# Kernel tuning notes

Measured on AMD Instinct MI355X. Metric: run time of the kernel, lower is better.

The kernel has to match this reference:

```python
import jax, jax.numpy as jnp
import numpy as np

N, E, D, H, OUT = 50000, 262144, 128, 256, 1
NUM_EXPERTS, TOP_K = 4, 1


def _mlp(x, w1, b1, w2, b2):
    return jnp.maximum(x @ w1 + b1, 0.0) @ w2 + b2


def setup_inputs() -> dict:
    key = jax.random.key(0)
    ks = jax.random.split(key, 16)
    def lin(k, fan_in, fan_out):
        bound = 1.0 / np.sqrt(fan_in)
        return jax.random.uniform(k, (fan_in, fan_out), jnp.float32, -bound, bound)
    return {
        "z": jax.random.normal(ks[0], (N, D), jnp.float32),
        "u": jax.random.randint(ks[1], (E,), 0, N, jnp.int64),
        "v": jax.random.randint(ks[2], (E,), 0, N, jnp.int64),
        "gate_w": lin(ks[3], 4 * D, NUM_EXPERTS),
        "gate_b": jnp.zeros((NUM_EXPERTS,), jnp.float32),
        "cat_w1": lin(ks[4], 2 * D, H), "cat_b1": jnp.zeros((H,), jnp.float32),
        "cat_w2": lin(ks[5], H, OUT), "cat_b2": jnp.zeros((OUT,), jnp.float32),
        "dist_w1": lin(ks[6], D, H), "dist_b1": jnp.zeros((H,), jnp.float32),
        "dist_w2": lin(ks[7], H, OUT), "dist_b2": jnp.zeros((OUT,), jnp.float32),
        "mul_w1": lin(ks[8], D, H), "mul_b1": jnp.zeros((H,), jnp.float32),
        "mul_w2": lin(ks[9], H, OUT), "mul_b2": jnp.zeros((OUT,), jnp.float32),
        "all_w1": lin(ks[10], 4 * D, H), "all_b1": jnp.zeros((H,), jnp.float32),
        "all_w2": lin(ks[11], H, OUT), "all_b2": jnp.zeros((OUT,), jnp.float32),
    }


def reference(z, u, v, gate_w, gate_b,
              cat_w1, cat_b1, cat_w2, cat_b2,
              dist_w1, dist_b1, dist_w2, dist_b2,
              mul_w1, mul_b1, mul_w2, mul_b2,
              all_w1, all_b1, all_w2, all_b2):
    z_u = z[u]                      # [E, D]
    z_v = z[v]                      # [E, D]
    z_cat = jnp.concatenate([z_u, z_v], axis=-1)        # [E, 2D]
    z_diff = jnp.abs(z_u - z_v)                         # [E, D]
    z_mul = z_u * z_v                                   # [E, D]
    edge_feat = jnp.concatenate([z_cat, z_diff, z_mul], axis=-1)  # [E, 4D]

    s1 = _mlp(z_cat, cat_w1, cat_b1, cat_w2, cat_b2)
    s2 = _mlp(z_diff, dist_w1, dist_b1, dist_w2, dist_b2)
    s3 = _mlp(z_mul, mul_w1, mul_b1, mul_w2, mul_b2)
    s4 = _mlp(edge_feat, all_w1, all_b1, all_w2, all_b2)
    scores = jnp.stack([s1, s2, s3, s4], axis=1)        # [E, 4, OUT]

    gate_logits = edge_feat @ gate_w + gate_b           # [E, 4]
    gate_probs = jax.nn.softmax(gate_logits, axis=-1)

    # top_k=1 with straight-through estimator (forward value == hard gate)
    topk_vals, topk_idx = jax.lax.top_k(gate_probs, TOP_K)
    hard_gate = jax.nn.one_hot(topk_idx[:, 0], NUM_EXPERTS, dtype=gate_probs.dtype) * topk_vals[:, :1]
    gate_st = hard_gate + gate_probs - jax.lax.stop_gradient(gate_probs)

    out = jnp.einsum("ek,eko->eo", gate_st, scores)     # [E, OUT]
    # dropout is identity in eval mode
    avg_expert_usage = gate_probs.mean(axis=0)
    aux_loss = (avg_expert_usage ** 2).sum() * NUM_EXPERTS
    return out, aux_loss
```

## Files before the change

kernel.cpp:

```cpp
#include <hip/hip_runtime.h>
#include <hip/hip_bf16.h>
#include <math.h>

#define N_NODES 50000
#define E_EDGES 262144
#define D_FEAT  128
#define H_HID   256
#define NEXP    4

typedef __attribute__((ext_vector_type(8))) short  short8;
typedef __attribute__((ext_vector_type(4))) float  floatx4;

#define W1B_OFF0 0
#define W1B_OFF1 65536
#define W1B_OFF2 98304
#define W1B_OFF3 131072
#define W1B_TOT  262144

__device__ __forceinline__ unsigned short f2bf(float f) {
    __hip_bfloat16 h = __float2bfloat16(f);
    return *reinterpret_cast<unsigned short*>(&h);
}

__global__ __launch_bounds__(256) void conv_kernel(
    const float* __restrict__ cw1, const float* __restrict__ dw1,
    const float* __restrict__ mw1, const float* __restrict__ aw1,
    unsigned short* __restrict__ w1b)
{
    int r = blockIdx.x;
    int n = threadIdx.x;
    const float* src; int k, off;
    if (r < 256)      { src = cw1; k = r;       off = W1B_OFF0; }
    else if (r < 384) { src = dw1; k = r - 256; off = W1B_OFF1; }
    else if (r < 512) { src = mw1; k = r - 384; off = W1B_OFF2; }
    else              { src = aw1; k = r - 512; off = W1B_OFF3; }
    w1b[off + (((k >> 3) * 256 + n) << 3) + (k & 7)] = f2bf(src[k * 256 + n]);
}

__global__ __launch_bounds__(256) void node_kernel(
    const float* __restrict__ z, const float* __restrict__ gw,
    double* __restrict__ nodeTab, double* __restrict__ gwd)
{
    int n = blockIdx.x * 256 + threadIdx.x;
    if (n < 128) {
        #pragma unroll
        for (int k = 0; k < 4; ++k) {
            gwd[n * 8 + k]     = (double)gw[4 * (256 + n) + k];
            gwd[n * 8 + 4 + k] = (double)gw[4 * (384 + n) + k];
        }
    }
    if (n >= N_NODES) return;

    const float4* zr = (const float4*)(z + (long)n * D_FEAT);
    double u0 = 0, u1 = 0, u2 = 0, u3 = 0;
    double v0 = 0, v1 = 0, v2 = 0, v3 = 0;
    for (int d4 = 0; d4 < D_FEAT / 4; ++d4) {
        float4 a = zr[d4];
        float av[4] = {a.x, a.y, a.z, a.w};
        #pragma unroll
        for (int j = 0; j < 4; ++j) {
            int d = d4 * 4 + j;
            const float4 g0 = *(const float4*)(gw + 4 * d);
            const float4 g1 = *(const float4*)(gw + 4 * (128 + d));
            double ad = (double)av[j];
            u0 += ad * (double)g0.x; u1 += ad * (double)g0.y;
            u2 += ad * (double)g0.z; u3 += ad * (double)g0.w;
            v0 += ad * (double)g1.x; v1 += ad * (double)g1.y;
            v2 += ad * (double)g1.z; v3 += ad * (double)g1.w;
        }
    }
    double* o = nodeTab + (long)n * 8;
    o[0] = u0; o[1] = u1; o[2] = u2; o[3] = u3;
    o[4] = v0; o[5] = v1; o[6] = v2; o[7] = v3;
}

__global__ __launch_bounds__(256) void gate_kernel(
    const float* __restrict__ z, const int* __restrict__ u, const int* __restrict__ v,
    const double* __restrict__ nodeTab, const double* __restrict__ gwd,
    const float* __restrict__ gb,
    float* __restrict__ probsum, unsigned* __restrict__ gcount,
    int* __restrict__ lists, float* __restrict__ pval)
{
    int tid  = threadIdx.x;
    int lane = tid & 63;
    int e    = blockIdx.x * 256 + tid;

    int ue = u[e], ve = v[e];
    const float4* zu4 = (const float4*)(z + (long)ue * D_FEAT);
    const float4* zv4 = (const float4*)(z + (long)ve * D_FEAT);
    const double* nu = nodeTab + (long)ue * 8;
    const double* nv = nodeTab + (long)ve * 8;

    double l0 = (double)gb[0] + nu[0] + nv[4];
    double l1 = (double)gb[1] + nu[1] + nv[5];
    double l2 = (double)gb[2] + nu[2] + nv[6];
    double l3 = (double)gb[3] + nu[3] + nv[7];

    for (int d4 = 0; d4 < D_FEAT / 4; ++d4) {
        float4 a = zu4[d4];
        float4 b = zv4[d4];
        float av[4] = {a.x, a.y, a.z, a.w};
        float bv[4] = {b.x, b.y, b.z, b.w};
        #pragma unroll
        for (int j = 0; j < 4; ++j) {
            int d = d4 * 4 + j;
            double ad = (double)fabsf(av[j] - bv[j]);
            double m  = (double)(av[j] * bv[j]);
            const double* gr = gwd + d * 8;
            l0 += ad * gr[0] + m * gr[4];
            l1 += ad * gr[1] + m * gr[5];
            l2 += ad * gr[2] + m * gr[6];
            l3 += ad * gr[3] + m * gr[7];
        }
    }

    int sel = 0;
    double lb = l0;
    if (l1 > lb) { lb = l1; sel = 1; }
    if (l2 > lb) { lb = l2; sel = 2; }
    if (l3 > lb) { lb = l3; sel = 3; }

    double mx = lb;
    float e0 = expf((float)(l0 - mx));
    float e1 = expf((float)(l1 - mx));
    float e2 = expf((float)(l2 - mx));
    float e3 = expf((float)(l3 - mx));
    float s  = e0 + e1 + e2 + e3;
    float inv = 1.0f / s;
    float p[4];
    p[0] = e0 * inv; p[1] = e1 * inv; p[2] = e2 * inv; p[3] = e3 * inv;
    float best = p[sel];

    __shared__ float s_ps[4];
    __shared__ int   s_cnt[4];
    __shared__ int   s_base[4];
    if (tid < 4) { s_ps[tid] = 0.0f; s_cnt[tid] = 0; }
    __syncthreads();

    float q0 = p[0], q1 = p[1], q2 = p[2], q3 = p[3];
    #pragma unroll
    for (int off = 32; off > 0; off >>= 1) {
        q0 += __shfl_down(q0, off);
        q1 += __shfl_down(q1, off);
        q2 += __shfl_down(q2, off);
        q3 += __shfl_down(q3, off);
    }
    if (lane == 0) {
        atomicAdd(&s_ps[0], q0); atomicAdd(&s_ps[1], q1);
        atomicAdd(&s_ps[2], q2); atomicAdd(&s_ps[3], q3);
    }

    unsigned long long lt = (lane == 0) ? 0ull : ((~0ull) >> (64 - lane));
    int mywb = 0, myrank = 0;
    #pragma unroll
    for (int k = 0; k < 4; ++k) {
        unsigned long long mask = __ballot(sel == k);
        if (mask) {
            int leader = (int)__ffsll((unsigned long long)mask) - 1;
            int wb = 0;
            if (lane == leader) wb = atomicAdd(&s_cnt[k], (int)__popcll(mask));
            wb = __shfl(wb, leader);
            if (sel == k) { mywb = wb; myrank = (int)__popcll(mask & lt); }
        }
    }
    __syncthreads();

    if (tid < 4) {
        s_base[tid] = (int)atomicAdd(&gcount[tid], (unsigned)s_cnt[tid]);
        atomicAdd(&probsum[tid], s_ps[tid]);
    }
    __syncthreads();

    int pos = s_base[sel] + mywb + myrank;
    lists[sel * E_EDGES + pos] = e;
    pval[e] = best;
}

#define FPAD 40
#define NCMAX 16

__global__ __launch_bounds__(256) void expert_kernel(
    const float* __restrict__ z, const int* __restrict__ u, const int* __restrict__ v,
    const unsigned short* __restrict__ w1b,
    const float* __restrict__ cb1, const float* __restrict__ cw2, const float* __restrict__ cb2,
    const float* __restrict__ db1, const float* __restrict__ dw2, const float* __restrict__ db2,
    const float* __restrict__ mb1, const float* __restrict__ mw2, const float* __restrict__ mb2,
    const float* __restrict__ ab1, const float* __restrict__ aw2, const float* __restrict__ ab2,
    const unsigned* __restrict__ gcount, const int* __restrict__ lists,
    const float* __restrict__ pval, float* __restrict__ out)
{
    int ex = blockIdx.y;
    const float *b1, *w2, *b2;
    int F, w1off;
    if (ex == 0)      { b1 = cb1; w2 = cw2; b2 = cb2; F = 256; w1off = W1B_OFF0; }
    else if (ex == 1) { b1 = db1; w2 = dw2; b2 = db2; F = 128; w1off = W1B_OFF1; }
    else if (ex == 2) { b1 = mb1; w2 = mw2; b2 = mb2; F = 128; w1off = W1B_OFF2; }
    else              { b1 = ab1; w2 = aw2; b2 = ab2; F = 512; w1off = W1B_OFF3; }

    unsigned cnt  = gcount[ex];
    unsigned tile = blockIdx.x * 32u;
    if (tile >= cnt) return;
    int nm = (int)min(32u, cnt - tile);

    __shared__ unsigned short featA[NCMAX][32][FPAD];
    __shared__ int   s_e[32], s_u[32], s_v[32];
    __shared__ float s_pv[32];
    __shared__ float red[4][32];

    int tid  = threadIdx.x;
    int wave = tid >> 6;
    int lane = tid & 63;
    int colA = lane & 15;
    int quad = lane >> 4;

    if (tid < 32) {
        int m = tid;
        int src = (m < nm) ? (int)(tile + m) : (int)tile;
        int e = lists[ex * E_EDGES + src];
        s_e[m] = e; s_u[m] = u[e]; s_v[m] = v[e]; s_pv[m] = pval[e];
    }
    __syncthreads();

    const short8* wB = (const short8*)(w1b + w1off);

    floatx4 acc[2][4];
    #pragma unroll
    for (int t = 0; t < 2; ++t)
        #pragma unroll
        for (int j = 0; j < 4; ++j)
            acc[t][j] = (floatx4)(0.0f);

    int fm = tid >> 3;
    int fk = (tid & 7) << 2;
    int nc = F >> 5;

    {
        const float* zu = z + (long)s_u[fm] * D_FEAT;
        const float* zv = z + (long)s_v[fm] * D_FEAT;
        for (int c = 0; c < nc; ++c) {
            int fg = c * 32 + fk;
            float4 val;
            if (ex == 0) {
                val = (fg < 128) ? *(const float4*)(zu + fg)
                                 : *(const float4*)(zv + fg - 128);
            } else if (ex == 1) {
                float4 a = *(const float4*)(zu + fg);
                float4 b = *(const float4*)(zv + fg);
                val.x = fabsf(a.x - b.x); val.y = fabsf(a.y - b.y);
                val.z = fabsf(a.z - b.z); val.w = fabsf(a.w - b.w);
            } else if (ex == 2) {
                float4 a = *(const float4*)(zu + fg);
                float4 b = *(const float4*)(zv + fg);
                val.x = a.x * b.x; val.y = a.y * b.y;
                val.z = a.z * b.z; val.w = a.w * b.w;
            } else {
                if (fg < 128) {
                    val = *(const float4*)(zu + fg);
                } else if (fg < 256) {
                    val = *(const float4*)(zv + fg - 128);
                } else if (fg < 384) {
                    float4 a = *(const float4*)(zu + fg - 256);
                    float4 b = *(const float4*)(zv + fg - 256);
                    val.x = fabsf(a.x - b.x); val.y = fabsf(a.y - b.y);
                    val.z = fabsf(a.z - b.z); val.w = fabsf(a.w - b.w);
                } else {
                    float4 a = *(const float4*)(zu + fg - 384);
                    float4 b = *(const float4*)(zv + fg - 384);
                    val.x = a.x * b.x; val.y = a.y * b.y;
                    val.z = a.z * b.z; val.w = a.w * b.w;
                }
            }
            ushort4 pk;
            pk.x = f2bf(val.x); pk.y = f2bf(val.y);
            pk.z = f2bf(val.z); pk.w = f2bf(val.w);
            *(ushort4*)(&featA[c][fm][fk]) = pk;
        }
    }
    __syncthreads();

    int nb = wave * 64 + colA;
    for (int c = 0; c < nc; ++c) {
        int g = c * 4 + quad;
        short8 bf0 = wB[g * 256 + nb +  0];
        short8 bf1 = wB[g * 256 + nb + 16];
        short8 bf2 = wB[g * 256 + nb + 32];
        short8 bf3 = wB[g * 256 + nb + 48];

        short8 a0 = *(const short8*)(&featA[c][colA][quad * 8]);
        short8 a1 = *(const short8*)(&featA[c][16 + colA][quad * 8]);

        acc[0][0] = __builtin_amdgcn_mfma_f32_16x16x32_bf16(a0, bf0, acc[0][0], 0, 0, 0);
        acc[1][0] = __builtin_amdgcn_mfma_f32_16x16x32_bf16(a1, bf0, acc[1][0], 0, 0, 0);
        acc[0][1] = __builtin_amdgcn_mfma_f32_16x16x32_bf16(a0, bf1, acc[0][1], 0, 0, 0);
        acc[1][1] = __builtin_amdgcn_mfma_f32_16x16x32_bf16(a1, bf1, acc[1][1], 0, 0, 0);
        acc[0][2] = __builtin_amdgcn_mfma_f32_16x16x32_bf16(a0, bf2, acc[0][2], 0, 0, 0);
        acc[1][2] = __builtin_amdgcn_mfma_f32_16x16x32_bf16(a1, bf2, acc[1][2], 0, 0, 0);
        acc[0][3] = __builtin_amdgcn_mfma_f32_16x16x32_bf16(a0, bf3, acc[0][3], 0, 0, 0);
        acc[1][3] = __builtin_amdgcn_mfma_f32_16x16x32_bf16(a1, bf3, acc[1][3], 0, 0, 0);
    }

    float b1v[4], w2v[4];
    #pragma unroll
    for (int j = 0; j < 4; ++j) {
        int h = wave * 64 + j * 16 + colA;
        b1v[j] = b1[h];
        w2v[j] = w2[h];
    }

    #pragma unroll
    for (int t = 0; t < 2; ++t) {
        #pragma unroll
        for (int r = 0; r < 4; ++r) {
            float s = 0.0f;
            #pragma unroll
            for (int j = 0; j < 4; ++j) {
                float h = acc[t][j][r] + b1v[j];
                s += fmaxf(h, 0.0f) * w2v[j];
            }
            s += __shfl_xor(s, 1);
            s += __shfl_xor(s, 2);
            s += __shfl_xor(s, 4);
            s += __shfl_xor(s, 8);
            if (colA == 0) {
                int m = 16 * t + quad * 4 + r;
                red[wave][m] = s;
            }
        }
    }
    __syncthreads();

    if (tid < 32) {
        int m = tid;
        if (m < nm) {
            float sc = red[0][m] + red[1][m] + red[2][m] + red[3][m] + b2[0];
            out[s_e[m]] = s_pv[m] * sc;
        }
    }
}

__global__ void aux_kernel(const float* __restrict__ probsum, float* __restrict__ out)
{
    if (threadIdx.x == 0 && blockIdx.x == 0) {
        float a = 0.0f;
        #pragma unroll
        for (int k = 0; k < 4; ++k) {
            float mean = probsum[k] * (1.0f / (float)E_EDGES);
            a += mean * mean;
        }
        out[E_EDGES] = a * (float)NEXP;
    }
}

extern "C" void kernel_launch(void* const* d_in, const int* in_sizes, int n_in,
                              void* d_out, int out_size, void* d_ws, size_t ws_size,
                              hipStream_t stream)
{
    const float* z   = (const float*)d_in[0];
    const int*   u   = (const int*)d_in[1];
    const int*   v   = (const int*)d_in[2];
    const float* gw  = (const float*)d_in[3];
    const float* gb  = (const float*)d_in[4];
    const float* cw1 = (const float*)d_in[5];
    const float* cb1 = (const float*)d_in[6];
    const float* cw2 = (const float*)d_in[7];
    const float* cb2 = (const float*)d_in[8];
    const float* dw1 = (const float*)d_in[9];
    const float* db1 = (const float*)d_in[10];
    const float* dw2 = (const float*)d_in[11];
    const float* db2 = (const float*)d_in[12];
    const float* mw1 = (const float*)d_in[13];
    const float* mb1 = (const float*)d_in[14];
    const float* mw2 = (const float*)d_in[15];
    const float* mb2 = (const float*)d_in[16];
    const float* aw1 = (const float*)d_in[17];
    const float* ab1 = (const float*)d_in[18];
    const float* aw2 = (const float*)d_in[19];
    const float* ab2 = (const float*)d_in[20];

    float* out = (float*)d_out;
    char*  ws  = (char*)d_ws;

    float*          probsum = (float*)ws;
    unsigned*       gcount  = (unsigned*)(ws + 16);
    int*            lists   = (int*)(ws + 32);
    float*          pval    = (float*)(ws + 32 + 16ll * E_EDGES);
    unsigned short* w1b     = (unsigned short*)(ws + 32 + 20ll * E_EDGES);
    double*         gwd     = (double*)(ws + 32 + 20ll * E_EDGES + 524288);
    double*         nodeTab = (double*)(ws + 32 + 20ll * E_EDGES + 524288 + 8192);

    hipMemsetAsync(d_ws, 0, 32, stream);

    conv_kernel<<<1024, 256, 0, stream>>>(cw1, dw1, mw1, aw1, w1b);

    node_kernel<<<(N_NODES + 255) / 256, 256, 0, stream>>>(z, gw, nodeTab, gwd);

    gate_kernel<<<E_EDGES / 256, 256, 0, stream>>>(z, u, v, nodeTab, gwd, gb,
                                                   probsum, gcount, lists, pval);

    aux_kernel<<<1, 64, 0, stream>>>(probsum, out);

    dim3 g2(E_EDGES / 32, 4);
    expert_kernel<<<g2, 256, 0, stream>>>(z, u, v, w1b,
                                          cb1, cw2, cb2,
                                          db1, dw2, db2,
                                          mb1, mw2, mb2,
                                          ab1, aw2, ab2,
                                          gcount, lists, pval, out);
}
```

Before: 350.6 us.

## Fuse prep kernels, split gate dot across thread pairs, enlarge expert tile to 64

Merges the weight-conversion and node-table kernels into one launch and folds the aux-loss computation into the expert kernel, removing two launches. The gate kernel now splits each edge's feature dot product across two threads with separate accumulators and combines them with a shuffle, for more parallelism and shorter dependency chains. The expert kernel moves from 32-edge to 64-edge tiles, staging features in chunks of 8 K-slices with extra barriers, so each weight fragment load is reused across twice as many MFMA rows. This raises register use (16 accumulators) and may lower occupancy, and it halves the number of expert blocks.

```diff
diff --git a/kernel.cpp b/kernel.cpp
--- a/kernel.cpp
+++ b/kernel.cpp
@@ -15,33 +15,34 @@
 #define W1B_OFF1 65536
 #define W1B_OFF2 98304
 #define W1B_OFF3 131072
-#define W1B_TOT  262144
 
 __device__ __forceinline__ unsigned short f2bf(float f) {
     __hip_bfloat16 h = __float2bfloat16(f);
     return *reinterpret_cast<unsigned short*>(&h);
 }
 
-__global__ __launch_bounds__(256) void conv_kernel(
+__global__ __launch_bounds__(256) void prep_kernel(
     const float* __restrict__ cw1, const float* __restrict__ dw1,
     const float* __restrict__ mw1, const float* __restrict__ aw1,
-    unsigned short* __restrict__ w1b)
-{
-    int r = blockIdx.x;
-    int n = threadIdx.x;
-    const float* src; int k, off;
-    if (r < 256)      { src = cw1; k = r;       off = W1B_OFF0; }
-    else if (r < 384) { src = dw1; k = r - 256; off = W1B_OFF1; }
-    else if (r < 512) { src = mw1; k = r - 384; off = W1B_OFF2; }
-    else              { src = aw1; k = r - 512; off = W1B_OFF3; }
-    w1b[off + (((k >> 3) * 256 + n) << 3) + (k & 7)] = f2bf(src[k * 256 + n]);
-}
-
-__global__ __launch_bounds__(256) void node_kernel(
+    unsigned short* __restrict__ w1b,
     const float* __restrict__ z, const float* __restrict__ gw,
     double* __restrict__ nodeTab, double* __restrict__ gwd)
 {
-    int n = blockIdx.x * 256 + threadIdx.x;
+    int bx  = blockIdx.x;
+    int tid = threadIdx.x;
+
+    if (bx < 1024) {
+        int r = bx, n = tid;
+        const float* src; int k, off;
+        if (r < 256)      { src = cw1; k = r;       off = W1B_OFF0; }
+        else if (r < 384) { src = dw1; k = r - 256; off = W1B_OFF1; }
+        else if (r < 512) { src = mw1; k = r - 384; off = W1B_OFF2; }
+        else              { src = aw1; k = r - 512; off = W1B_OFF3; }
+        w1b[off + (((k >> 3) * 256 + n) << 3) + (k & 7)] = f2bf(src[k * 256 + n]);
+        return;
+    }
+
+    int n = (bx - 1024) * 256 + tid;
     if (n < 128) {
         #pragma unroll
         for (int k = 0; k < 4; ++k) {
@@ -83,36 +84,48 @@
 {
     int tid  = threadIdx.x;
     int lane = tid & 63;
-    int e    = blockIdx.x * 256 + tid;
+    int half = tid & 1;
+    int e    = blockIdx.x * 128 + (tid >> 1);
 
     int ue = u[e], ve = v[e];
-    const float4* zu4 = (const float4*)(z + (long)ue * D_FEAT);
-    const float4* zv4 = (const float4*)(z + (long)ve * D_FEAT);
-    const double* nu = nodeTab + (long)ue * 8;
-    const double* nv = nodeTab + (long)ve * 8;
-
-    double l0 = (double)gb[0] + nu[0] + nv[4];
-    double l1 = (double)gb[1] + nu[1] + nv[5];
-    double l2 = (double)gb[2] + nu[2] + nv[6];
-    double l3 = (double)gb[3] + nu[3] + nv[7];
-
-    for (int d4 = 0; d4 < D_FEAT / 4; ++d4) {
+    const float4* zu4 = (const float4*)(z + (long)ue * D_FEAT) + half * 16;
+    const float4* zv4 = (const float4*)(z + (long)ve * D_FEAT) + half * 16;
+    const double* grb = gwd + (long)(half * 64) * 8;
+
+    double la0 = 0, la1 = 0, la2 = 0, la3 = 0;
+    double lm0 = 0, lm1 = 0, lm2 = 0, lm3 = 0;
+
+    #pragma unroll 4
+    for (int d4 = 0; d4 < 16; ++d4) {
         float4 a = zu4[d4];
         float4 b = zv4[d4];
         float av[4] = {a.x, a.y, a.z, a.w};
         float bv[4] = {b.x, b.y, b.z, b.w};
         #pragma unroll
         for (int j = 0; j < 4; ++j) {
-            int d = d4 * 4 + j;
             double ad = (double)fabsf(av[j] - bv[j]);
             double m  = (double)(av[j] * bv[j]);
-            const double* gr = gwd + d * 8;
-            l0 += ad * gr[0] + m * gr[4];
-            l1 += ad * gr[1] + m * gr[5];
-            l2 += ad * gr[2] + m * gr[6];
-            l3 += ad * gr[3] + m * gr[7];
-        }
-    }
+            const double* gr = grb + (d4 * 4 + j) * 8;
+            la0 += ad * gr[0]; lm0 += m * gr[4];
+            la1 += ad * gr[1]; lm1 += m * gr[5];
+            la2 += ad * gr[2]; lm2 += m * gr[6];
+            la3 += ad * gr[3]; lm3 += m * gr[7];
+        }
+    }
+
+    double l0 = la0 + lm0, l1 = la1 + lm1, l2 = la2 + lm2, l3 = la3 + lm3;
+    if (half == 0) {
+        const double* nu = nodeTab + (long)ue * 8;
+        const double* nv = nodeTab + (long)ve * 8;
+        l0 += (double)gb[0] + nu[0] + nv[4];
+        l1 += (double)gb[1] + nu[1] + nv[5];
+        l2 += (double)gb[2] + nu[2] + nv[6];
+        l3 += (double)gb[3] + nu[3] + nv[7];
+    }
+    l0 += __shfl_xor(l0, 1);
+    l1 += __shfl_xor(l1, 1);
+    l2 += __shfl_xor(l2, 1);
+    l3 += __shfl_xor(l3, 1);
 
     int sel = 0;
     double lb = l0;
@@ -120,12 +133,11 @@
     if (l2 > lb) { lb = l2; sel = 2; }
     if (l3 > lb) { lb = l3; sel = 3; }
 
-    double mx = lb;
-    float e0 = expf((float)(l0 - mx));
-    float e1 = expf((float)(l1 - mx));
-    float e2 = expf((float)(l2 - mx));
-    float e3 = expf((float)(l3 - mx));
-    float s  = e0 + e1 + e2 + e3;
+    float e0 = expf((float)(l0 - lb));
+    float e1 = expf((float)(l1 - lb));
+    float e2 = expf((float)(l2 - lb));
+    float e3 = expf((float)(l3 - lb));
+    float s   = e0 + e1 + e2 + e3;
     float inv = 1.0f / s;
     float p[4];
     p[0] = e0 * inv; p[1] = e1 * inv; p[2] = e2 * inv; p[3] = e3 * inv;
@@ -137,7 +149,10 @@
     if (tid < 4) { s_ps[tid] = 0.0f; s_cnt[tid] = 0; }
     __syncthreads();
 
-    float q0 = p[0], q1 = p[1], q2 = p[2], q3 = p[3];
+    float q0 = half ? 0.0f : p[0];
+    float q1 = half ? 0.0f : p[1];
+    float q2 = half ? 0.0f : p[2];
+    float q3 = half ? 0.0f : p[3];
     #pragma unroll
     for (int off = 32; off > 0; off >>= 1) {
         q0 += __shfl_down(q0, off);
@@ -150,17 +165,18 @@
         atomicAdd(&s_ps[2], q2); atomicAdd(&s_ps[3], q3);
     }
 
+    const unsigned long long EV = 0x5555555555555555ull;
     unsigned long long lt = (lane == 0) ? 0ull : ((~0ull) >> (64 - lane));
     int mywb = 0, myrank = 0;
     #pragma unroll
     for (int k = 0; k < 4; ++k) {
-        unsigned long long mask = __ballot(sel == k);
+        unsigned long long mask = __ballot(sel == k) & EV;
         if (mask) {
             int leader = (int)__ffsll((unsigned long long)mask) - 1;
             int wb = 0;
             if (lane == leader) wb = atomicAdd(&s_cnt[k], (int)__popcll(mask));
             wb = __shfl(wb, leader);
-            if (sel == k) { mywb = wb; myrank = (int)__popcll(mask & lt); }
+            if (half == 0 && sel == k) { mywb = wb; myrank = (int)__popcll(mask & lt); }
         }
     }
     __syncthreads();
@@ -171,13 +187,46 @@
     }
     __syncthreads();
 
-    int pos = s_base[sel] + mywb + myrank;
-    lists[sel * E_EDGES + pos] = e;
-    pval[e] = best;
+    if (half == 0) {
+        int pos = s_base[sel] + mywb + myrank;
+        lists[sel * E_EDGES + pos] = e;
+        pval[e] = best;
+    }
 }
 
 #define FPAD 40
-#define NCMAX 16
+
+__device__ __forceinline__ float4 edge_feat4(int ex, const float* zu, const float* zv, int fg)
+{
+    if (ex == 0) {
+        return (fg < 128) ? *(const float4*)(zu + fg)
+                          : *(const float4*)(zv + fg - 128);
+    } else if (ex == 1) {
+        float4 a = *(const float4*)(zu + fg);
+        float4 b = *(const float4*)(zv + fg);
+        return make_float4(fabsf(a.x - b.x), fabsf(a.y - b.y),
+                           fabsf(a.z - b.z), fabsf(a.w - b.w));
+    } else if (ex == 2) {
+        float4 a = *(const float4*)(zu + fg);
+        float4 b = *(const float4*)(zv + fg);
+        return make_float4(a.x * b.x, a.y * b.y, a.z * b.z, a.w * b.w);
+    } else {
+        if (fg < 128) {
+            return *(const float4*)(zu + fg);
+        } else if (fg < 256) {
+            return *(const float4*)(zv + fg - 128);
+        } else if (fg < 384) {
+            float4 a = *(const float4*)(zu + fg - 256);
+            float4 b = *(const float4*)(zv + fg - 256);
+            return make_float4(fabsf(a.x - b.x), fabsf(a.y - b.y),
+                               fabsf(a.z - b.z), fabsf(a.w - b.w));
+        } else {
+            float4 a = *(const float4*)(zu + fg - 384);
+            float4 b = *(const float4*)(zv + fg - 384);
+            return make_float4(a.x * b.x, a.y * b.y, a.z * b.z, a.w * b.w);
+        }
+    }
+}
 
 __global__ __launch_bounds__(256) void expert_kernel(
     const float* __restrict__ z, const int* __restrict__ u, const int* __restrict__ v,
@@ -187,8 +236,21 @@
     const float* __restrict__ mb1, const float* __restrict__ mw2, const float* __restrict__ mb2,
     const float* __restrict__ ab1, const float* __restrict__ aw2, const float* __restrict__ ab2,
     const unsigned* __restrict__ gcount, const int* __restrict__ lists,
-    const float* __restrict__ pval, float* __restrict__ out)
+    const float* __restrict__ pval, const float* __restrict__ probsum,
+    float* __restrict__ out)
 {
+    int tid = threadIdx.x;
+
+    if (blockIdx.x == 0 && blockIdx.y == 0 && tid == 0) {
+        float a = 0.0f;
+        #pragma unroll
+        for (int k = 0; k < 4; ++k) {
+            float mean = probsum[k] * (1.0f / (float)E_EDGES);
+            a += mean * mean;
+        }
+        out[E_EDGES] = a * (float)NEXP;
+    }
+
     int ex = blockIdx.y;
     const float *b1, *w2, *b2;
     int F, w1off;
@@ -198,22 +260,21 @@
     else              { b1 = ab1; w2 = aw2; b2 = ab2; F = 512; w1off = W1B_OFF3; }
 
     unsigned cnt  = gcount[ex];
-    unsigned tile = blockIdx.x * 32u;
+    unsigned tile = blockIdx.x * 64u;
     if (tile >= cnt) return;
-    int nm = (int)min(32u, cnt - tile);
-
-    __shared__ unsigned short featA[NCMAX][32][FPAD];
-    __shared__ int   s_e[32], s_u[32], s_v[32];
-    __shared__ float s_pv[32];
-    __shared__ float red[4][32];
-
-    int tid  = threadIdx.x;
+    int nm = (int)min(64u, cnt - tile);
+
+    __shared__ unsigned short featA[8][64][FPAD];
+    __shared__ int   s_e[64], s_u[64], s_v[64];
+    __shared__ float s_pv[64];
+    __shared__ float red[4][64];
+
     int wave = tid >> 6;
     int lane = tid & 63;
     int colA = lane & 15;
     int quad = lane >> 4;
 
-    if (tid < 32) {
+    if (tid < 64) {
         int m = tid;
         int src = (m < nm) ? (int)(tile + m) : (int)tile;
         int e = lists[ex * E_EDGES + src];
@@ -223,80 +284,67 @@
 
     const short8* wB = (const short8*)(w1b + w1off);
 
-    floatx4 acc[2][4];
+    floatx4 acc[4][4];
     #pragma unroll
-    for (int t = 0; t < 2; ++t)
+    for (int t = 0; t < 4; ++t)
         #pragma unroll
         for (int j = 0; j < 4; ++j)
             acc[t][j] = (floatx4)(0.0f);
 
-    int fm = tid >> 3;
-    int fk = (tid & 7) << 2;
-    int nc = F >> 5;
-
-    {
-        const float* zu = z + (long)s_u[fm] * D_FEAT;
-        const float* zv = z + (long)s_v[fm] * D_FEAT;
-        for (int c = 0; c < nc; ++c) {
-            int fg = c * 32 + fk;
-            float4 val;
-            if (ex == 0) {
-                val = (fg < 128) ? *(const float4*)(zu + fg)
-                                 : *(const float4*)(zv + fg - 128);
-            } else if (ex == 1) {
-                float4 a = *(const float4*)(zu + fg);
-                float4 b = *(const float4*)(zv + fg);
-                val.x = fabsf(a.x - b.x); val.y = fabsf(a.y - b.y);
-                val.z = fabsf(a.z - b.z); val.w = fabsf(a.w - b.w);
-            } else if (ex == 2) {
-                float4 a = *(const float4*)(zu + fg);
-                float4 b = *(const float4*)(zv + fg);
-                val.x = a.x * b.x; val.y = a.y * b.y;
-                val.z = a.z * b.z; val.w = a.w * b.w;
-            } else {
-                if (fg < 128) {
-                    val = *(const float4*)(zu + fg);
-                } else if (fg < 256) {
-                    val = *(const float4*)(zv + fg - 128);
-                } else if (fg < 384) {
-                    float4 a = *(const float4*)(zu + fg - 256);
-                    float4 b = *(const float4*)(zv + fg - 256);
-                    val.x = fabsf(a.x - b.x); val.y = fabsf(a.y - b.y);
-                    val.z = fabsf(a.z - b.z); val.w = fabsf(a.w - b.w);
-                } else {
-                    float4 a = *(const float4*)(zu + fg - 384);
-                    float4 b = *(const float4*)(zv + fg - 384);
-                    val.x = a.x * b.x; val.y = a.y * b.y;
-                    val.z = a.z * b.z; val.w = a.w * b.w;
-                }
-            }
-            ushort4 pk;
-            pk.x = f2bf(val.x); pk.y = f2bf(val.y);
-            pk.z = f2bf(val.z); pk.w = f2bf(val.w);
-            *(ushort4*)(&featA[c][fm][fk]) = pk;
-        }
-    }
-    __syncthreads();
-
+    int fm  = tid >> 2;
+    int fk8 = (tid & 3) << 3;
+    int nc  = F >> 5;
+    const float* zu = z + (long)s_u[fm] * D_FEAT;
+    const float* zv = z + (long)s_v[fm] * D_FEAT;
     int nb = wave * 64 + colA;
-    for (int c = 0; c < nc; ++c) {
-        int g = c * 4 + quad;
-        short8 bf0 = wB[g * 256 + nb +  0];
-        short8 bf1 = wB[g * 256 + nb + 16];
-        short8 bf2 = wB[g * 256 + nb + 32];
-        short8 bf3 = wB[g * 256 + nb + 48];
-
-        short8 a0 = *(const short8*)(&featA[c][colA][quad * 8]);
-        short8 a1 = *(const short8*)(&featA[c][16 + colA][quad * 8]);
-
-        acc[0][0] = __builtin_amdgcn_mfma_f32_16x16x32_bf16(a0, bf0, acc[0][0], 0, 0, 0);
-        acc[1][0] = __builtin_amdgcn_mfma_f32_16x16x32_bf16(a1, bf0, acc[1][0], 0, 0, 0);
-        acc[0][1] = __builtin_amdgcn_mfma_f32_16x16x32_bf16(a0, bf1, acc[0][1], 0, 0, 0);
-        acc[1][1] = __builtin_amdgcn_mfma_f32_16x16x32_bf16(a1, bf1, acc[1][1], 0, 0, 0);
-        acc[0][2] = __builtin_amdgcn_mfma_f32_16x16x32_bf16(a0, bf2, acc[0][2], 0, 0, 0);
-        acc[1][2] = __builtin_amdgcn_mfma_f32_16x16x32_bf16(a1, bf2, acc[1][2], 0, 0, 0);
-        acc[0][3] = __builtin_amdgcn_mfma_f32_16x16x32_bf16(a0, bf3, acc[0][3], 0, 0, 0);
-        acc[1][3] = __builtin_amdgcn_mfma_f32_16x16x32_bf16(a1, bf3, acc[1][3], 0, 0, 0);
+
+    for (int c0 = 0; c0 < nc; c0 += 8) {
+        int cend = min(8, nc - c0);
+        if (c0) __syncthreads();
+
+        for (int cc = 0; cc < cend; ++cc) {
+            int fg = (c0 + cc) * 32 + fk8;
+            float4 v0 = edge_feat4(ex, zu, zv, fg);
+            float4 v1 = edge_feat4(ex, zu, zv, fg + 4);
+            ushort4 pk0, pk1;
+            pk0.x = f2bf(v0.x); pk0.y = f2bf(v0.y);
+            pk0.z = f2bf(v0.z); pk0.w = f2bf(v0.w);
+            pk1.x = f2bf(v1.x); pk1.y = f2bf(v1.y);
+            pk1.z = f2bf(v1.z); pk1.w = f2bf(v1.w);
+            *(ushort4*)(&featA[cc][fm][fk8])     = pk0;
+            *(ushort4*)(&featA[cc][fm][fk8 + 4]) = pk1;
+        }
+        __syncthreads();
+
+        for (int cc = 0; cc < cend; ++cc) {
+            int g = (c0 + cc) * 4 + quad;
+            short8 bf0 = wB[g * 256 + nb +  0];
+            short8 bf1 = wB[g * 256 + nb + 16];
+            short8 bf2 = wB[g * 256 + nb + 32];
+            short8 bf3 = wB[g * 256 + nb + 48];
+
+            short8 a0 = *(const short8*)(&featA[cc][colA][quad * 8]);
+            short8 a1 = *(const short8*)(&featA[cc][16 + colA][quad * 8]);
+            short8 a2 = *(const short8*)(&featA[cc][32 + colA][quad * 8]);
+            short8 a3 = *(const short8*)(&featA[cc][48 + colA][quad * 8]);
+
+            acc[0][0] = __builtin_amdgcn_mfma_f32_16x16x32_bf16(a0, bf0, acc[0][0], 0, 0, 0);
+            acc[1][0] = __builtin_amdgcn_mfma_f32_16x16x32_bf16(a1, bf0, acc[1][0], 0, 0, 0);
+            acc[2][0] = __builtin_amdgcn_mfma_f32_16x16x32_bf16(a2, bf0, acc[2][0], 0, 0, 0);
+            acc[3][0] = __builtin_amdgcn_mfma_f32_16x16x32_bf16(a3, bf0, acc[3][0], 0, 0, 0);
+            acc[0][1] = __builtin_amdgcn_mfma_f32_16x16x32_bf16(a0, bf1, acc[0][1], 0, 0, 0);
+            acc[1][1] = __builtin_amdgcn_mfma_f32_16x16x32_bf16(a1, bf1, acc[1][1], 0, 0, 0);
+            acc[2][1] = __builtin_amdgcn_mfma_f32_16x16x32_bf16(a2, bf1, acc[2][1], 0, 0, 0);
+            acc[3][1] = __builtin_amdgcn_mfma_f32_16x16x32_bf16(a3, bf1, acc[3][1], 0, 0, 0);
+            acc[0][2] = __builtin_amdgcn_mfma_f32_16x16x32_bf16(a0, bf2, acc[0][2], 0, 0, 0);
+            acc[1][2] = __builtin_amdgcn_mfma_f32_16x16x32_bf16(a1, bf2, acc[1][2], 0, 0, 0);
+            acc[2][2] = __builtin_amdgcn_mfma_f32_16x16x32_bf16(a2, bf2, acc[2][2], 0, 0, 0);
+            acc[3][2] = __builtin_amdgcn_mfma_f32_16x16x32_bf16(a3, bf2, acc[3][2], 0, 0, 0);
+            acc[0][3] = __builtin_amdgcn_mfma_f32_16x16x32_bf16(a0, bf3, acc[0][3], 0, 0, 0);
+            acc[1][3] = __builtin_amdgcn_mfma_f32_16x16x32_bf16(a1, bf3, acc[1][3], 0, 0, 0);
+            acc[2][3] = __builtin_amdgcn_mfma_f32_16x16x32_bf16(a2, bf3, acc[2][3], 0, 0, 0);
+            acc[3][3] = __builtin_amdgcn_mfma_f32_16x16x32_bf16(a3, bf3, acc[3][3], 0, 0, 0);
+        }
     }
 
     float b1v[4], w2v[4];
@@ -308,7 +356,7 @@
     }
 
     #pragma unroll
-    for (int t = 0; t < 2; ++t) {
+    for (int t = 0; t < 4; ++t) {
         #pragma unroll
         for (int r = 0; r < 4; ++r) {
             float s = 0.0f;
@@ -329,25 +377,12 @@
     }
     __syncthreads();
 
-    if (tid < 32) {
+    if (tid < 64) {
         int m = tid;
         if (m < nm) {
             float sc = red[0][m] + red[1][m] + red[2][m] + red[3][m] + b2[0];
             out[s_e[m]] = s_pv[m] * sc;
         }
-    }
-}
-
-__global__ void aux_kernel(const float* __restrict__ probsum, float* __restrict__ out)
-{
-    if (threadIdx.x == 0 && blockIdx.x == 0) {
-        float a = 0.0f;
-        #pragma unroll
-        for (int k = 0; k < 4; ++k) {
-            float mean = probsum[k] * (1.0f / (float)E_EDGES);
-            a += mean * mean;
-        }
-        out[E_EDGES] = a * (float)NEXP;
     }
 }
 
@@ -390,20 +425,17 @@
 
     hipMemsetAsync(d_ws, 0, 32, stream);
 
-    conv_kernel<<<1024, 256, 0, stream>>>(cw1, dw1, mw1, aw1, w1b);
-
-    node_kernel<<<(N_NODES + 255) / 256, 256, 0, stream>>>(z, gw, nodeTab, gwd);
-
-    gate_kernel<<<E_EDGES / 256, 256, 0, stream>>>(z, u, v, nodeTab, gwd, gb,
+    prep_kernel<<<1024 + (N_NODES + 255) / 256, 256, 0, stream>>>(
+        cw1, dw1, mw1, aw1, w1b, z, gw, nodeTab, gwd);
+
+    gate_kernel<<<E_EDGES / 128, 256, 0, stream>>>(z, u, v, nodeTab, gwd, gb,
                                                    probsum, gcount, lists, pval);
 
-    aux_kernel<<<1, 64, 0, stream>>>(probsum, out);
-
-    dim3 g2(E_EDGES / 32, 4);
+    dim3 g2(E_EDGES / 64, 4);
     expert_kernel<<<g2, 256, 0, stream>>>(z, u, v, w1b,
                                           cb1, cw2, cb2,
                                           db1, dw2, db2,
                                           mb1, mw2, mb2,
                                           ab1, aw2, ab2,
-                                          gcount, lists, pval, out);
-}
+                                          gcount, lists, pval, probsum, out);
+}
```

Result: slower. 385.2 us (+9.9%).
